# Performance work log

Hardware: AMD Instinct MI355X
Metric: run time of the kernel (lower is better)

## Reference

```python
import jax, jax.numpy as jnp
import numpy as np

N, R, A, F = 6000, 5, 8, 128
K, O = 2, 128
RADIUS = 0.028
ROT_DELTA = 1


def _kernel_matrix(n_radial, n_angular, radius):
    # polar grid of kernel vertices -> cartesian, shape (R, A, 2)
    r = radius * (np.arange(1, n_radial + 1, dtype=np.float64) / n_radial)
    theta = 2.0 * np.pi * np.arange(n_angular, dtype=np.float64) / n_angular
    x = r[:, None] * np.cos(theta)[None, :]
    y = r[:, None] * np.sin(theta)[None, :]
    return np.stack([x, y], axis=-1)


def _interp_coefficients(n_radial, n_angular, radius):
    # Gaussian interpolation weights w(rho_a,theta_b,rho_c,theta_d), normalized,
    # reshaped to (R, A, R*A) as in _configure_patch_operator.
    kv = _kernel_matrix(n_radial, n_angular, radius)           # (R, A, 2)
    flat = kv.reshape(-1, 2)                                   # (R*A, 2)
    d2 = ((kv[:, :, None, :] - flat[None, None, :, :]) ** 2).sum(-1)  # (R, A, R*A)
    sigma = radius / n_radial
    w = np.exp(-d2 / (2.0 * sigma * sigma))
    w = w / w.sum(axis=-1, keepdims=True)
    return w.astype(np.float32)


def setup_inputs() -> dict:
    key = jax.random.key(0)
    k1, k2, k3, k4, k5 = jax.random.split(key, 5)
    mesh_signal = jax.random.normal(k1, (N, F), dtype=jnp.float32)
    # barycentric coords: channel 0 = vertex indices (stored as float), channel 1 = weights summing to 1
    idx = jax.random.randint(k2, (N, R, A, 3), 0, N).astype(jnp.float32)
    w = jax.random.uniform(k3, (N, R, A, 3), dtype=jnp.float32)
    w = w / w.sum(axis=-1, keepdims=True)
    bary_coordinates = jnp.stack([idx, w], axis=-1)            # (N, R, A, 3, 2)
    kernel_weights = jax.random.normal(k4, (R, A, K, O, F), dtype=jnp.float32) * 0.05
    bias = jax.random.normal(k5, (K, O), dtype=jnp.float32) * 0.05
    interp_coeffs = jnp.asarray(_interp_coefficients(R, A, RADIUS))  # (R, A, R*A)
    return {"mesh_signal": mesh_signal, "bary_coordinates": bary_coordinates,
            "kernel_weights": kernel_weights, "bias": bias, "interp_coeffs": interp_coeffs}


def reference(mesh_signal, bary_coordinates, kernel_weights, bias, interp_coeffs):
    # 1) gather + barycentric interpolation
    idx = bary_coordinates[..., 0].astype(jnp.int32)           # (N, R, A, 3)
    w = bary_coordinates[..., 1]                               # (N, R, A, 3)
    collected = mesh_signal[idx]                               # (N, R, A, 3, F)
    sig = jnp.sum(w[..., None] * collected, axis=-2)           # (N, R, A, F)
    # 2) patch operator: F_x @ I[a,b]
    flat = sig.reshape(-1, R * A, F)                           # (N, R*A, F)
    patched = jnp.einsum('nqf,raq->nraf', flat, interp_coeffs)  # (N, R, A, F)
    # 3) rotation-shifted fold (splits=1 -> single chunk; splits don't change math)
    outs = []
    for rot in range(0, A, ROT_DELTA):
        rolled = jnp.roll(patched, shift=rot, axis=2)          # (N, R, A, F)
        s = jnp.einsum('nraf,rakof->nko', rolled, kernel_weights) + (R * A) * bias  # (N, K, O)
        outs.append(jax.nn.relu(s).sum(axis=1))                # (N, O)
    return jnp.stack(outs, axis=1)                             # (N, n_rotations, O)
```

## Files before the change

### kernel.cpp

```cpp
#include <hip/hip_runtime.h>
#include <hip/hip_bf16.h>


#define N_PTS 6000
#define RR 5
#define AA 8
#define FF 128
#define OO 128
#define QQ 40
#define KD2 1280
#define SIG_BLOCKS 750
#define W2_BLOCKS 128
#define CCQ 0.70710678118654752f
#define RT2 1.41421356237309515f

#define AHS ((size_t)N_PTS * KD2)
#define BHS ((size_t)512 * KD2)

typedef __bf16 bf16_t;
typedef __bf16 bf16x4 __attribute__((ext_vector_type(4)));
typedef __bf16 bf16x8 __attribute__((ext_vector_type(8)));
typedef float f32x4 __attribute__((ext_vector_type(4)));

#define GLOAD_LDS16(g, l)                                              \
  __builtin_amdgcn_global_load_lds(                                    \
      (const __attribute__((address_space(1))) void*)(g),              \
      (__attribute__((address_space(3))) void*)(l), 16, 0, 0)

#define DFT8V(xx, c, X0, X4, Xr1, Xi1, Xr2, Xi2, Xr3, Xi3)             \
  {                                                                    \
    const float s0_ = xx[0][c] + xx[4][c], s1_ = xx[1][c] + xx[5][c];  \
    const float s2_ = xx[2][c] + xx[6][c], s3_ = xx[3][c] + xx[7][c];  \
    const float d0_ = xx[0][c] - xx[4][c], d1_ = xx[1][c] - xx[5][c];  \
    const float d2_ = xx[2][c] - xx[6][c], d3_ = xx[3][c] - xx[7][c];  \
    const float e_ = CCQ * (d1_ - d3_), o_ = CCQ * (d1_ + d3_);        \
    X0 = (s0_ + s2_) + (s1_ + s3_);                                    \
    X4 = (s0_ + s2_) - (s1_ + s3_);                                    \
    Xr2 = s0_ - s2_; Xi2 = s3_ - s1_;                                  \
    Xr1 = d0_ + e_;  Xi1 = -(o_ + d2_);                                \
    Xr3 = d0_ - e_;  Xi3 = d2_ - o_;                                   \
  }

#define PACK4(dst, X)                                                  \
  {                                                                    \
    bf16x4 pv_;                                                        \
    pv_[0] = (bf16_t)X[0]; pv_[1] = (bf16_t)X[1];                      \
    pv_[2] = (bf16_t)X[2]; pv_[3] = (bf16_t)X[3];                      \
    *(bf16x4*)(dst) = pv_;                                             \
  }

__global__ __launch_bounds__(256) void prep_fft_kernel(
    const float* __restrict__ mesh, const float* __restrict__ bary,
    const float* __restrict__ kw, const float* __restrict__ interp,
    bf16_t* __restrict__ Ahat, bf16_t* __restrict__ Bhat) {
  __shared__ float sI[RR * AA * QQ];
  const int bx = blockIdx.x;
  const int tid = threadIdx.x;

  if (bx < SIG_BLOCKS) {
    const int slot = tid >> 5;
    const int l = tid & 31;
    const int n = bx * 8 + slot;
    const float* bn = bary + (size_t)n * (QQ * 6);
    bf16_t* an = Ahat + (size_t)n * KD2 + l * 4;
#pragma unroll
    for (int rho = 0; rho < RR; ++rho) {
      float x[8][4];
#pragma unroll
      for (int a = 0; a < 8; ++a) {
        const float* b = bn + (rho * 8 + a) * 6;
        const float2 p0 = *(const float2*)(b);
        const float2 p1 = *(const float2*)(b + 2);
        const float2 p2 = *(const float2*)(b + 4);
        const float4 v0 =
            *(const float4*)(mesh + (size_t)((int)p0.x) * FF + l * 4);
        const float4 v1 =
            *(const float4*)(mesh + (size_t)((int)p1.x) * FF + l * 4);
        const float4 v2 =
            *(const float4*)(mesh + (size_t)((int)p2.x) * FF + l * 4);
        x[a][0] = p0.y * v0.x + p1.y * v1.x + p2.y * v2.x;
        x[a][1] = p0.y * v0.y + p1.y * v1.y + p2.y * v2.y;
        x[a][2] = p0.y * v0.z + p1.y * v1.z + p2.y * v2.z;
        x[a][3] = p0.y * v0.w + p1.y * v1.w + p2.y * v2.w;
      }
      float X0[4], X4[4], Xr1[4], Xi1[4], Xr2[4], Xi2[4], Xr3[4], Xi3[4];
#pragma unroll
      for (int c = 0; c < 4; ++c)
        DFT8V(x, c, X0[c], X4[c], Xr1[c], Xi1[c], Xr2[c], Xi2[c], Xr3[c],
              Xi3[c]);
      bf16_t* dst = an + rho * 256;
      PACK4(dst, X0);                  PACK4(dst + 128, X4);
      PACK4(dst + AHS, Xr1);           PACK4(dst + AHS + 128, Xi1);
      PACK4(dst + 2 * AHS, Xr2);       PACK4(dst + 2 * AHS + 128, Xi2);
      PACK4(dst + 3 * AHS, Xr3);       PACK4(dst + 3 * AHS + 128, Xi3);
    }
  } else {
    const int j = (bx - SIG_BLOCKS) * 2 + (tid >> 7);
    const int f = tid & 127;
    for (int i = tid; i < RR * AA * QQ; i += 256) sI[i] = interp[i];
    __syncthreads();
    const int o = (j >> 1) & 127;
    const int k = j & 1;
    float acc[QQ];
#pragma unroll
    for (int q = 0; q < QQ; ++q) acc[q] = 0.f;
    for (int r = 0; r < RR; ++r) {
      for (int a = 0; a < AA; ++a) {
        const float kv =
            kw[((size_t)((r * AA + a) * 2 + k) * OO + o) * FF + f];
        const float4* ip = (const float4*)(sI + (r * AA + a) * QQ);
#pragma unroll
        for (int q4 = 0; q4 < QQ / 4; ++q4) {
          const float4 w4 = ip[q4];
          acc[q4 * 4 + 0] += w4.x * kv;
          acc[q4 * 4 + 1] += w4.y * kv;
          acc[q4 * 4 + 2] += w4.z * kv;
          acc[q4 * 4 + 3] += w4.w * kv;
        }
      }
    }
    const float SC = 0.125f;
    bf16_t* b1p = Bhat + (size_t)j * KD2 + f;
    bf16_t* b2p = Bhat + (size_t)(256 + j) * KD2 + f;
#pragma unroll
    for (int rho = 0; rho < RR; ++rho) {
      float xx[8][1];
#pragma unroll
      for (int a = 0; a < 8; ++a) xx[a][0] = acc[rho * 8 + a];
      float Y0, Y4, Yr1, Yi1, Yr2, Yi2, Yr3, Yi3;
      DFT8V(xx, 0, Y0, Y4, Yr1, Yi1, Yr2, Yi2, Yr3, Yi3);
      const int off = rho * 256;
      b1p[off] = (bf16_t)(Y0 * SC);        b1p[off + 128] = (bf16_t)0.f;
      b2p[off] = (bf16_t)0.f;              b2p[off + 128] = (bf16_t)(Y4 * SC);
      b1p[BHS + off] = (bf16_t)(Yr1 * SC);
      b1p[BHS + off + 128] = (bf16_t)(Yi1 * SC);
      b2p[BHS + off] = (bf16_t)(Yi1 * SC);
      b2p[BHS + off + 128] = (bf16_t)(-Yr1 * SC);
      b1p[2 * BHS + off] = (bf16_t)(Yr2 * SC);
      b1p[2 * BHS + off + 128] = (bf16_t)(Yi2 * SC);
      b2p[2 * BHS + off] = (bf16_t)(Yi2 * SC);
      b2p[2 * BHS + off + 128] = (bf16_t)(-Yr2 * SC);
      b1p[3 * BHS + off] = (bf16_t)(Yr3 * SC);
      b1p[3 * BHS + off + 128] = (bf16_t)(Yi3 * SC);
      b2p[3 * BHS + off] = (bf16_t)(Yi3 * SC);
      b2p[3 * BHS + off + 128] = (bf16_t)(-Yr3 * SC);
    }
  }
}

__global__ __launch_bounds__(256, 3) void gemm_fused_fft_kernel(
    const bf16_t* __restrict__ Ahat, const bf16_t* __restrict__ Bhat,
    const float* __restrict__ bias, float* __restrict__ out) {
  const int L = blockIdx.x;
  const int xcd = L & 7;
  const int t = L >> 3;
  const int g = xcd + 8 * (t >> 4);
  const int jt = t & 15;
  const int m0 = g * 128;
  if (m0 >= N_PTS) return;
  const int j0 = jt * 16;

  __shared__ bf16_t As[128 * 64];
  __shared__ bf16_t Bs[32 * 64];
  const int tid = threadIdx.x;
  const int wave = tid >> 6;
  const int lane = tid & 63;
  const int quad = lane >> 4;
  const int tl = lane & 15;
  const int wm = wave * 32;
  const int srow = lane >> 3;
  const int sc = (lane & 7) ^ srow;

  const int crow = wave * 8;
  const int colbase = (crow < 16) ? (j0 + crow) : (256 + j0 + (crow - 16));
  const int gcol = colbase + srow;

  static const float CF[4][8] = {
      {1, 1, 1, 1, 1, 1, 1, 1},
      {2, RT2, 0, -RT2, -2, -RT2, 0, RT2},
      {2, 0, -2, 0, 2, 0, -2, 0},
      {2, -RT2, 0, RT2, -2, RT2, 0, -RT2}};
  static const float SF[4][8] = {
      {1, -1, 1, -1, 1, -1, 1, -1},
      {0, -RT2, -2, -RT2, 0, RT2, 2, RT2},
      {0, -2, 0, 2, 0, -2, 0, 2},
      {0, -RT2, 2, -RT2, 0, RT2, -2, RT2}};

  f32x4 oacc[8][2];
#pragma unroll
  for (int rot = 0; rot < 8; ++rot)
#pragma unroll
    for (int mm = 0; mm < 2; ++mm) oacc[rot][mm] = {0.f, 0.f, 0.f, 0.f};

#pragma unroll
  for (int b = 0; b < 4; ++b) {
    const bf16_t* A = Ahat + (size_t)b * AHS;
    const bf16_t* B = Bhat + (size_t)b * BHS;
    f32x4 z[2][2];
#pragma unroll
    for (int mm = 0; mm < 2; ++mm)
#pragma unroll
      for (int cc = 0; cc < 2; ++cc) z[mm][cc] = {0.f, 0.f, 0.f, 0.f};

    for (int kk = 0; kk < KD2; kk += 64) {
      __syncthreads();
#pragma unroll
      for (int i = 0; i < 4; ++i) {
        const int row = wave * 32 + i * 8;
        int gm = m0 + row + srow;
        gm = gm < N_PTS ? gm : (N_PTS - 1);
        GLOAD_LDS16(A + (size_t)gm * KD2 + kk + sc * 8, As + row * 64);
      }
      GLOAD_LDS16(B + (size_t)gcol * KD2 + kk + sc * 8, Bs + crow * 64);
      __syncthreads();
#pragma unroll
      for (int ks = 0; ks < 2; ++ks) {
        const int ch = (((ks * 4 + quad) ^ (tl & 7)) * 8);
        bf16x8 af[2], bfr[2];
        af[0] = *(const bf16x8*)(As + (wm + tl) * 64 + ch);
        af[1] = *(const bf16x8*)(As + (wm + 16 + tl) * 64 + ch);
        bfr[0] = *(const bf16x8*)(Bs + tl * 64 + ch);
        bfr[1] = *(const bf16x8*)(Bs + (16 + tl) * 64 + ch);
#pragma unroll
        for (int mm = 0; mm < 2; ++mm)
#pragma unroll
          for (int cc = 0; cc < 2; ++cc)
            z[mm][cc] = __builtin_amdgcn_mfma_f32_16x16x32_bf16(
                af[mm], bfr[cc], z[mm][cc], 0, 0, 0);
      }
    }
#pragma unroll
    for (int rot = 0; rot < 8; ++rot) {
      const float cf = CF[b][rot], sf = SF[b][rot];
#pragma unroll
      for (int mm = 0; mm < 2; ++mm)
#pragma unroll
        for (int r = 0; r < 4; ++r)
          oacc[rot][mm][r] += cf * z[mm][0][r] + sf * z[mm][1][r];
    }
  }

  const int j = j0 + tl;
  const float bb = 40.0f * bias[((j & 1) << 7) | (j >> 1)];
  const int o = j >> 1;
#pragma unroll
  for (int rot = 0; rot < 8; ++rot)
#pragma unroll
    for (int mm = 0; mm < 2; ++mm)
#pragma unroll
      for (int r = 0; r < 4; ++r) {
        const int mrow = m0 + wm + mm * 16 + quad * 4 + r;
        float v = oacc[rot][mm][r] + bb;
        v = v > 0.f ? v : 0.f;
        const float vs = v + __shfl_xor(v, 1, 64);
        if (((lane & 1) == 0) && (mrow < N_PTS))
          out[(size_t)mrow * 1024 + rot * 128 + o] = vs;
      }
}

extern "C" void kernel_launch(void* const* d_in, const int* in_sizes, int n_in,
                              void* d_out, int out_size, void* d_ws,
                              size_t ws_size, hipStream_t stream) {
  const float* mesh = (const float*)d_in[0];
  const float* bary = (const float*)d_in[1];
  const float* kw = (const float*)d_in[2];
  const float* bias = (const float*)d_in[3];
  const float* interp = (const float*)d_in[4];
  float* out = (float*)d_out;

  bf16_t* Ahat = (bf16_t*)d_ws;
  bf16_t* Bhat = (bf16_t*)((char*)d_ws + 4 * AHS * 2);

  prep_fft_kernel<<<SIG_BLOCKS + W2_BLOCKS, 256, 0, stream>>>(
      mesh, bary, kw, interp, Ahat, Bhat);
  gemm_fused_fft_kernel<<<768, 256, 0, stream>>>(Ahat, Bhat, bias, out);
}
```

Before: 163.0 us.

## Split fused FFT-bin GEMM into per-bin GEMM grid plus separate fold kernel

The single GEMM kernel that looped over four frequency bins and folded the results in registers becomes two kernels. The first is a GEMM launched over a 2D grid with one bin per grid row, which has four times as many blocks and a higher occupancy hint. It writes the raw real and imaginary partial products to a float workspace Z. A new fold kernel then reads Z and applies the inverse-FFT coefficients, bias, ReLU and the K-sum. This gains parallelism and lower register pressure, but adds a round trip of about 24 MB through global memory and one extra launch.

New measurement: 167.3 us. +2.7%, slower.

```diff
diff --git a/kernel.cpp b/kernel.cpp
--- a/kernel.cpp
+++ b/kernel.cpp
@@ -3,6 +3,7 @@
 
 
 #define N_PTS 6000
+#define MR 6016
 #define RR 5
 #define AA 8
 #define FF 128
@@ -148,10 +149,11 @@
   }
 }
 
-__global__ __launch_bounds__(256, 3) void gemm_fused_fft_kernel(
+__global__ __launch_bounds__(256, 6) void gemm_bin_kernel(
     const bf16_t* __restrict__ Ahat, const bf16_t* __restrict__ Bhat,
-    const float* __restrict__ bias, float* __restrict__ out) {
+    float* __restrict__ Z) {
   const int L = blockIdx.x;
+  const int bin = blockIdx.y;
   const int xcd = L & 7;
   const int t = L >> 3;
   const int g = xcd + 8 * (t >> 4);
@@ -159,6 +161,8 @@
   const int m0 = g * 128;
   if (m0 >= N_PTS) return;
   const int j0 = jt * 16;
+  const bf16_t* A = Ahat + (size_t)bin * AHS;
+  const bf16_t* B = Bhat + (size_t)bin * BHS;
 
   __shared__ bf16_t As[128 * 64];
   __shared__ bf16_t Bs[32 * 64];
@@ -175,6 +179,60 @@
   const int colbase = (crow < 16) ? (j0 + crow) : (256 + j0 + (crow - 16));
   const int gcol = colbase + srow;
 
+  f32x4 z[2][2];
+#pragma unroll
+  for (int mm = 0; mm < 2; ++mm)
+#pragma unroll
+    for (int cc = 0; cc < 2; ++cc) z[mm][cc] = {0.f, 0.f, 0.f, 0.f};
+
+  for (int kk = 0; kk < KD2; kk += 64) {
+    __syncthreads();
+#pragma unroll
+    for (int i = 0; i < 4; ++i) {
+      const int row = wave * 32 + i * 8;
+      int gm = m0 + row + srow;
+      gm = gm < N_PTS ? gm : (N_PTS - 1);
+      GLOAD_LDS16(A + (size_t)gm * KD2 + kk + sc * 8, As + row * 64);
+    }
+    GLOAD_LDS16(B + (size_t)gcol * KD2 + kk + sc * 8, Bs + crow * 64);
+    __syncthreads();
+#pragma unroll
+    for (int ks = 0; ks < 2; ++ks) {
+      const int ch = (((ks * 4 + quad) ^ (tl & 7)) * 8);
+      bf16x8 af[2], bfr[2];
+      af[0] = *(const bf16x8*)(As + (wm + tl) * 64 + ch);
+      af[1] = *(const bf16x8*)(As + (wm + 16 + tl) * 64 + ch);
+      bfr[0] = *(const bf16x8*)(Bs + tl * 64 + ch);
+      bfr[1] = *(const bf16x8*)(Bs + (16 + tl) * 64 + ch);
+#pragma unroll
+      for (int mm = 0; mm < 2; ++mm)
+#pragma unroll
+        for (int cc = 0; cc < 2; ++cc)
+          z[mm][cc] = __builtin_amdgcn_mfma_f32_16x16x32_bf16(
+              af[mm], bfr[cc], z[mm][cc], 0, 0, 0);
+    }
+  }
+
+#pragma unroll
+  for (int cc = 0; cc < 2; ++cc) {
+    float* zp = Z + ((size_t)(bin * 2 + cc) * MR) * 256 + j0 + tl;
+#pragma unroll
+    for (int mm = 0; mm < 2; ++mm)
+#pragma unroll
+      for (int r = 0; r < 4; ++r) {
+        const int mrow = m0 + wm + mm * 16 + quad * 4 + r;
+        zp[(size_t)mrow * 256] = z[mm][cc][r];
+      }
+  }
+}
+
+__global__ __launch_bounds__(256) void fold_kernel(
+    const float* __restrict__ Z, const float* __restrict__ bias,
+    float* __restrict__ out) {
+  const int T = blockIdx.x * 256 + threadIdx.x;
+  const int m = T >> 7;
+  const int o = T & 127;
+
   static const float CF[4][8] = {
       {1, 1, 1, 1, 1, 1, 1, 1},
       {2, RT2, 0, -RT2, -2, -RT2, 0, RT2},
@@ -186,76 +244,33 @@
       {0, -2, 0, 2, 0, -2, 0, 2},
       {0, -RT2, 2, -RT2, 0, RT2, -2, RT2}};
 
-  f32x4 oacc[8][2];
-#pragma unroll
-  for (int rot = 0; rot < 8; ++rot)
-#pragma unroll
-    for (int mm = 0; mm < 2; ++mm) oacc[rot][mm] = {0.f, 0.f, 0.f, 0.f};
-
+  float re[4][2], im[4][2];
 #pragma unroll
   for (int b = 0; b < 4; ++b) {
-    const bf16_t* A = Ahat + (size_t)b * AHS;
-    const bf16_t* B = Bhat + (size_t)b * BHS;
-    f32x4 z[2][2];
-#pragma unroll
-    for (int mm = 0; mm < 2; ++mm)
-#pragma unroll
-      for (int cc = 0; cc < 2; ++cc) z[mm][cc] = {0.f, 0.f, 0.f, 0.f};
-
-    for (int kk = 0; kk < KD2; kk += 64) {
-      __syncthreads();
-#pragma unroll
-      for (int i = 0; i < 4; ++i) {
-        const int row = wave * 32 + i * 8;
-        int gm = m0 + row + srow;
-        gm = gm < N_PTS ? gm : (N_PTS - 1);
-        GLOAD_LDS16(A + (size_t)gm * KD2 + kk + sc * 8, As + row * 64);
-      }
-      GLOAD_LDS16(B + (size_t)gcol * KD2 + kk + sc * 8, Bs + crow * 64);
-      __syncthreads();
-#pragma unroll
-      for (int ks = 0; ks < 2; ++ks) {
-        const int ch = (((ks * 4 + quad) ^ (tl & 7)) * 8);
-        bf16x8 af[2], bfr[2];
-        af[0] = *(const bf16x8*)(As + (wm + tl) * 64 + ch);
-        af[1] = *(const bf16x8*)(As + (wm + 16 + tl) * 64 + ch);
-        bfr[0] = *(const bf16x8*)(Bs + tl * 64 + ch);
-        bfr[1] = *(const bf16x8*)(Bs + (16 + tl) * 64 + ch);
-#pragma unroll
-        for (int mm = 0; mm < 2; ++mm)
-#pragma unroll
-          for (int cc = 0; cc < 2; ++cc)
-            z[mm][cc] = __builtin_amdgcn_mfma_f32_16x16x32_bf16(
-                af[mm], bfr[cc], z[mm][cc], 0, 0, 0);
-      }
-    }
-#pragma unroll
-    for (int rot = 0; rot < 8; ++rot) {
-      const float cf = CF[b][rot], sf = SF[b][rot];
-#pragma unroll
-      for (int mm = 0; mm < 2; ++mm)
-#pragma unroll
-        for (int r = 0; r < 4; ++r)
-          oacc[rot][mm][r] += cf * z[mm][0][r] + sf * z[mm][1][r];
-    }
-  }
-
-  const int j = j0 + tl;
-  const float bb = 40.0f * bias[((j & 1) << 7) | (j >> 1)];
-  const int o = j >> 1;
-#pragma unroll
-  for (int rot = 0; rot < 8; ++rot)
-#pragma unroll
-    for (int mm = 0; mm < 2; ++mm)
-#pragma unroll
-      for (int r = 0; r < 4; ++r) {
-        const int mrow = m0 + wm + mm * 16 + quad * 4 + r;
-        float v = oacc[rot][mm][r] + bb;
-        v = v > 0.f ? v : 0.f;
-        const float vs = v + __shfl_xor(v, 1, 64);
-        if (((lane & 1) == 0) && (mrow < N_PTS))
-          out[(size_t)mrow * 1024 + rot * 128 + o] = vs;
-      }
+    const float2 vr = *(const float2*)(
+        Z + ((size_t)(b * 2) * MR + m) * 256 + 2 * o);
+    const float2 vi = *(const float2*)(
+        Z + ((size_t)(b * 2 + 1) * MR + m) * 256 + 2 * o);
+    re[b][0] = vr.x; re[b][1] = vr.y;
+    im[b][0] = vi.x; im[b][1] = vi.y;
+  }
+  const float b0 = 40.0f * bias[o];
+  const float b1 = 40.0f * bias[128 + o];
+  float* op = out + (size_t)m * 1024 + o;
+#pragma unroll
+  for (int rot = 0; rot < 8; ++rot) {
+    float c0 = 0.f, c1 = 0.f;
+#pragma unroll
+    for (int b = 0; b < 4; ++b) {
+      c0 += CF[b][rot] * re[b][0] + SF[b][rot] * im[b][0];
+      c1 += CF[b][rot] * re[b][1] + SF[b][rot] * im[b][1];
+    }
+    float v0 = c0 + b0;
+    float v1 = c1 + b1;
+    v0 = v0 > 0.f ? v0 : 0.f;
+    v1 = v1 > 0.f ? v1 : 0.f;
+    op[rot * 128] = v0 + v1;
+  }
 }
 
 extern "C" void kernel_launch(void* const* d_in, const int* in_sizes, int n_in,
@@ -270,8 +285,11 @@
 
   bf16_t* Ahat = (bf16_t*)d_ws;
   bf16_t* Bhat = (bf16_t*)((char*)d_ws + 4 * AHS * 2);
+  float* Z =
+      (float*)((char*)d_ws + 4 * AHS * 2 + 4 * BHS * 2);
 
   prep_fft_kernel<<<SIG_BLOCKS + W2_BLOCKS, 256, 0, stream>>>(
       mesh, bary, kw, interp, Ahat, Bhat);
-  gemm_fused_fft_kernel<<<768, 256, 0, stream>>>(Ahat, Bhat, bias, out);
-}
+  gemm_bin_kernel<<<dim3(768, 4), 256, 0, stream>>>(Ahat, Bhat, Z);
+  fold_kernel<<<3000, 256, 0, stream>>>(Z, bias, out);
+}
```
